# Performance work log

Measured on AMD Instinct MI355X. Metric: run time of the kernel, lower is better.

## Reference

```python
import jax, jax.numpy as jnp
import numpy as np

NUM_NODES = 50000
NUM_HYPEREDGES = 20000
NNZ = 1600000
IN_DIM = 256
OUT_DIM = 128


def setup_inputs() -> dict:
    key = jax.random.key(0)
    k1, k2, k3, k4, k5 = jax.random.split(key, 5)
    x = jax.random.normal(k1, (NUM_NODES, IN_DIM), dtype=jnp.float32)
    node_idx = jax.random.randint(k2, (NNZ,), 0, NUM_NODES)
    edge_idx = jax.random.randint(k3, (NNZ,), 0, NUM_HYPEREDGES)
    hyperedge_index = jnp.stack([node_idx, edge_idx], axis=0)  # [2, nnz]
    # glorot-style init for HypergraphConv's internal Linear (bias=False)
    scale = np.sqrt(6.0 / (IN_DIM + OUT_DIM)).astype(np.float32)
    lin_weight = jax.random.uniform(k4, (IN_DIM, OUT_DIM), dtype=jnp.float32,
                                    minval=-scale, maxval=scale)
    bias = jnp.zeros((OUT_DIM,), dtype=jnp.float32)
    return {"x_node_features": x, "lin_weight": lin_weight, "bias": bias,
            "hyperedge_index": hyperedge_index}


def reference(x_node_features, lin_weight, bias, hyperedge_index):
    src = hyperedge_index[0]   # node ids   [nnz]
    edge = hyperedge_index[1]  # hyperedge ids [nnz]
    ones = jnp.ones_like(src, dtype=x_node_features.dtype)

    # X Theta
    xw = x_node_features @ lin_weight  # [N, F_out]

    # D^{-1}: node degree (hyperedge weights default to 1)
    deg_n = jax.ops.segment_sum(ones, src, num_segments=NUM_NODES)
    d_inv = jnp.where(deg_n > 0, 1.0 / deg_n, 0.0)
    # B^{-1}: hyperedge cardinality
    deg_e = jax.ops.segment_sum(ones, edge, num_segments=NUM_HYPEREDGES)
    b_inv = jnp.where(deg_e > 0, 1.0 / deg_e, 0.0)

    # node -> hyperedge: m_e = B_e^{-1} * sum_{i in e} (X Theta)_i
    m_e = jax.ops.segment_sum(xw[src], edge, num_segments=NUM_HYPEREDGES)
    m_e = m_e * b_inv[:, None]  # [E, F_out]

    # hyperedge -> node: out_i = D_i^{-1} * sum_{e ni i} m_e
    out = jax.ops.segment_sum(m_e[edge], src, num_segments=NUM_NODES)
    out = out * d_inv[:, None] + bias  # [N, F_out]

    # ReLU + mean pool over nodes
    return jnp.mean(jax.nn.relu(out), axis=0)  # [F_out]
```

## Files before the change

kernel.cpp:

```cpp
#include <hip/hip_runtime.h>

#define NUM_N 50000
#define NUM_E 20000
#define IN_DIM 256
#define OUT_DIM 128
#define NBE 1250
#define NBN 1563
#define NCLS 8
#define ECAPC 256
#define NCAPC 192
#define SCAT_CHUNK 4096
#define NGEMM 782
#define XSCALE 16.0f

typedef unsigned short ushort_t;
typedef unsigned int uint_t;
typedef __attribute__((ext_vector_type(8))) short short8_t;
typedef __attribute__((ext_vector_type(4))) float f32x4_t;

__device__ __forceinline__ int clamp8(int q) { return min(max(q, -127), 127); }
__device__ __forceinline__ int lo8(uint_t u) { return (int)(signed char)(u & 0xff); }
__device__ __forceinline__ int hi8(uint_t u) { return ((int)(short)(ushort_t)u) >> 8; }
__device__ __forceinline__ ushort_t f2bf(float f) {
    uint_t u = __float_as_uint(f);
    u += 0x7fffu + ((u >> 16) & 1u);
    return (ushort_t)(u >> 16);
}

__global__ void init_kernel(int* __restrict__ gcur_e, int* __restrict__ gcur_n,
                            float* __restrict__ macc) {
    int t = blockIdx.x * 1024 + threadIdx.x;
    if (t < NCLS * NBE) gcur_e[t] = t * ECAPC;
    if (t < NCLS * NBN) gcur_n[t] = t * NCAPC;
    if (t < 128) macc[t] = 0.f;
}

__global__ __launch_bounds__(256) void gemm_scatter_kernel(
        const float* __restrict__ x, const float* __restrict__ w,
        char* __restrict__ xw, int nrows,
        const int* __restrict__ node_idx, const int* __restrict__ edge_idx, int nnz,
        int* __restrict__ gcur_e, int* __restrict__ gcur_n,
        uint_t* __restrict__ stag_e, uint_t* __restrict__ stag_n) {
    __shared__ int smem[5632];
    int tid = threadIdx.x;

    if (blockIdx.x >= NGEMM) {
        int* lh    = smem;
        int* lbase = smem + 2813;
        int cls = blockIdx.x & (NCLS - 1);
        int bid = blockIdx.x - NGEMM;
        int nblk = gridDim.x - NGEMM;
        for (int cbase = bid * SCAT_CHUNK; cbase < nnz; cbase += nblk * SCAT_CHUNK) {
            int cend = min(cbase + SCAT_CHUNK, nnz);
            for (int i = tid; i < NBE + NBN; i += 256) lh[i] = 0;
            __syncthreads();
            for (int i = cbase + tid; i < cend; i += 256) {
                atomicAdd(&lh[edge_idx[i] >> 4], 1);
                atomicAdd(&lh[NBE + (node_idx[i] >> 5)], 1);
            }
            __syncthreads();
            for (int i = tid; i < NBE; i += 256) {
                int c = lh[i];
                lbase[i] = c ? atomicAdd(&gcur_e[cls * NBE + i], c) : 0;
            }
            for (int i = tid; i < NBN; i += 256) {
                int c = lh[NBE + i];
                lbase[NBE + i] = c ? atomicAdd(&gcur_n[cls * NBN + i], c) : 0;
            }
            __syncthreads();
            for (int i = tid; i < NBE + NBN; i += 256) lh[i] = 0;
            __syncthreads();
            for (int i = cbase + tid; i < cend; i += 256) {
                int v = node_idx[i];
                int e = edge_idx[i];
                uint_t pk = ((uint_t)v << 16) | (uint_t)e;
                int be = e >> 4;
                int bn = v >> 5;
                int pe = lbase[be] + atomicAdd(&lh[be], 1);
                if (pe < (cls * NBE + be + 1) * ECAPC) stag_e[pe] = pk;
                int pn = lbase[NBE + bn] + atomicAdd(&lh[NBE + bn], 1);
                if (pn < (cls * NBN + bn + 1) * NCAPC) stag_n[pn] = pk;
            }
            __syncthreads();
        }
        return;
    }

    ushort_t* Wt = (ushort_t*)smem;
    int lane = tid & 63;
    int wv = tid >> 6;
    int R = blockIdx.x * 64 + wv * 16;
    int fr = lane & 15;
    int kb = lane >> 4;
    f32x4_t acc[8];
#pragma unroll
    for (int c = 0; c < 8; ++c) acc[c] = (f32x4_t){0.f, 0.f, 0.f, 0.f};
    int arow = min(R + fr, nrows - 1);
    const float* ap = x + (size_t)arow * IN_DIM + kb * 8;

    for (int k0 = 0; k0 < IN_DIM; k0 += 32) {
        __syncthreads();
        {
            int tk = tid >> 3;
            int tc = (tid & 7) * 16;
            const float* wp = w + (size_t)(k0 + tk) * OUT_DIM + tc;
            float4 w0 = *(const float4*)(wp + 0);
            float4 w1 = *(const float4*)(wp + 4);
            float4 w2 = *(const float4*)(wp + 8);
            float4 w3 = *(const float4*)(wp + 12);
            float wvv[16] = {w0.x, w0.y, w0.z, w0.w, w1.x, w1.y, w1.z, w1.w,
                             w2.x, w2.y, w2.z, w2.w, w3.x, w3.y, w3.z, w3.w};
#pragma unroll
            for (int i = 0; i < 16; ++i)
                Wt[(tc + i) * 40 + tk] = f2bf(wvv[i]);
        }
        __syncthreads();
        float4 a0 = *(const float4*)(ap + k0);
        float4 a1 = *(const float4*)(ap + k0 + 4);
        short8_t af;
        af[0] = (short)f2bf(a0.x); af[1] = (short)f2bf(a0.y);
        af[2] = (short)f2bf(a0.z); af[3] = (short)f2bf(a0.w);
        af[4] = (short)f2bf(a1.x); af[5] = (short)f2bf(a1.y);
        af[6] = (short)f2bf(a1.z); af[7] = (short)f2bf(a1.w);
#pragma unroll
        for (int c = 0; c < 8; ++c) {
            short8_t bf = *(short8_t*)&Wt[(c * 16 + fr) * 40 + kb * 8];
            acc[c] = __builtin_amdgcn_mfma_f32_16x16x32_bf16(af, bf, acc[c], 0, 0, 0);
        }
    }
#pragma unroll
    for (int c = 0; c < 8; ++c) {
#pragma unroll
        for (int j = 0; j < 4; ++j) {
            int row = R + kb * 4 + j;
            if (row < nrows) {
                int q = clamp8(__float2int_rn(acc[c][j] * XSCALE));
                xw[(size_t)row * OUT_DIM + c * 16 + fr] = (char)q;
            }
        }
    }
}

__global__ __launch_bounds__(256) void edge_agg_kernel(const uint_t* __restrict__ stag_e,
                                                       const int* __restrict__ gcur_e,
                                                       const ushort_t* __restrict__ xw16,
                                                       ushort_t* __restrict__ me16) {
    __shared__ int acc[16 * 128];
    __shared__ int cnt[16];
    int tid = threadIdx.x;
    int lane = tid & 63;
    int wid = tid >> 6;
    int b = blockIdx.x;
    for (int i = tid; i < 16 * 128; i += 256) acc[i] = 0;
    if (tid < 16) cnt[tid] = 0;
    __syncthreads();
    for (int cls = 0; cls < NCLS; ++cls) {
        int idx = cls * NBE + b;
        int beg = idx * ECAPC;
        int end = min(gcur_e[idx], beg + ECAPC);
        int cb = beg + wid * 16;
        for (; cb + 16 <= end; cb += 64) {
            uint4 pa = *(const uint4*)&stag_e[cb];
            uint4 pb = *(const uint4*)&stag_e[cb + 4];
            uint4 pc = *(const uint4*)&stag_e[cb + 8];
            uint4 pd = *(const uint4*)&stag_e[cb + 12];
            uint_t pk[16] = {pa.x, pa.y, pa.z, pa.w, pb.x, pb.y, pb.z, pb.w,
                             pc.x, pc.y, pc.z, pc.w, pd.x, pd.y, pd.z, pd.w};
            uint_t u[16];
#pragma unroll
            for (int j = 0; j < 16; ++j)
                u[j] = xw16[(size_t)(pk[j] >> 16) * 64 + lane];
#pragma unroll
            for (int j = 0; j < 16; ++j) {
                int r = (pk[j] & 15) * 128;
                atomicAdd(&acc[r + lane],      lo8(u[j]));
                atomicAdd(&acc[r + 64 + lane], hi8(u[j]));
            }
            if (lane == 0) {
#pragma unroll
                for (int j = 0; j < 16; ++j) atomicAdd(&cnt[pk[j] & 15], 1);
            }
        }
        if (cb < end) {
            int m = end - cb;
            uint4 pa = *(const uint4*)&stag_e[cb];
            uint4 pb = *(const uint4*)&stag_e[cb + 4];
            uint4 pc = *(const uint4*)&stag_e[cb + 8];
            uint4 pd = *(const uint4*)&stag_e[cb + 12];
            uint_t pk[16] = {pa.x, pa.y, pa.z, pa.w, pb.x, pb.y, pb.z, pb.w,
                             pc.x, pc.y, pc.z, pc.w, pd.x, pd.y, pd.z, pd.w};
            uint_t u[16];
#pragma unroll
            for (int j = 0; j < 16; ++j)
                u[j] = xw16[(size_t)(pk[j] >> 16) * 64 + lane];
#pragma unroll
            for (int j = 0; j < 16; ++j) {
                bool ok = j < m;
                int r = (pk[j] & 15) * 128;
                atomicAdd(&acc[r + lane],      ok ? lo8(u[j]) : 0);
                atomicAdd(&acc[r + 64 + lane], ok ? hi8(u[j]) : 0);
            }
            if (lane == 0) {
#pragma unroll
                for (int j = 0; j < 16; ++j)
                    if (j < m) atomicAdd(&cnt[pk[j] & 15], 1);
            }
        }
    }
    __syncthreads();
    for (int r = wid; r < 16; r += 4) {
        int e = b * 16 + r;
        int c = cnt[r];
        float f = c ? 4.0f / (float)c : 0.f;
        int q0 = clamp8(__float2int_rn((float)acc[r * 128 + lane] * f));
        int q1 = clamp8(__float2int_rn((float)acc[r * 128 + 64 + lane] * f));
        me16[(size_t)e * 64 + lane] = (ushort_t)((q0 & 0xff) | ((q1 & 0xff) << 8));
    }
}

__global__ __launch_bounds__(256) void node_agg_kernel(const uint_t* __restrict__ stag_n,
                                                       const int* __restrict__ gcur_n,
                                                       const ushort_t* __restrict__ me16,
                                                       const float* __restrict__ bias,
                                                       float* __restrict__ mean_acc) {
    __shared__ int acc[32 * 128];
    __shared__ int cnt[32];
    int tid = threadIdx.x;
    int lane = tid & 63;
    int wid = tid >> 6;
    int b = blockIdx.x;
    for (int i = tid; i < 32 * 128; i += 256) acc[i] = 0;
    if (tid < 32) cnt[tid] = 0;
    __syncthreads();
    for (int cls = 0; cls < NCLS; ++cls) {
        int idx = cls * NBN + b;
        int beg = idx * NCAPC;
        int end = min(gcur_n[idx], beg + NCAPC);
        int cb = beg + wid * 16;
        for (; cb + 16 <= end; cb += 64) {
            uint4 pa = *(const uint4*)&stag_n[cb];
            uint4 pb = *(const uint4*)&stag_n[cb + 4];
            uint4 pc = *(const uint4*)&stag_n[cb + 8];
            uint4 pd = *(const uint4*)&stag_n[cb + 12];
            uint_t pk[16] = {pa.x, pa.y, pa.z, pa.w, pb.x, pb.y, pb.z, pb.w,
                             pc.x, pc.y, pc.z, pc.w, pd.x, pd.y, pd.z, pd.w};
            uint_t u[16];
#pragma unroll
            for (int j = 0; j < 16; ++j)
                u[j] = me16[(size_t)(pk[j] & 0xffff) * 64 + lane];
#pragma unroll
            for (int j = 0; j < 16; ++j) {
                int r = ((pk[j] >> 16) & 31) * 128;
                atomicAdd(&acc[r + lane],      lo8(u[j]));
                atomicAdd(&acc[r + 64 + lane], hi8(u[j]));
            }
            if (lane == 0) {
#pragma unroll
                for (int j = 0; j < 16; ++j) atomicAdd(&cnt[(pk[j] >> 16) & 31], 1);
            }
        }
        if (cb < end) {
            int m = end - cb;
            uint4 pa = *(const uint4*)&stag_n[cb];
            uint4 pb = *(const uint4*)&stag_n[cb + 4];
            uint4 pc = *(const uint4*)&stag_n[cb + 8];
            uint4 pd = *(const uint4*)&stag_n[cb + 12];
            uint_t pk[16] = {pa.x, pa.y, pa.z, pa.w, pb.x, pb.y, pb.z, pb.w,
                             pc.x, pc.y, pc.z, pc.w, pd.x, pd.y, pd.z, pd.w};
            uint_t u[16];
#pragma unroll
            for (int j = 0; j < 16; ++j)
                u[j] = me16[(size_t)(pk[j] & 0xffff) * 64 + lane];
#pragma unroll
            for (int j = 0; j < 16; ++j) {
                bool ok = j < m;
                int r = ((pk[j] >> 16) & 31) * 128;
                atomicAdd(&acc[r + lane],      ok ? lo8(u[j]) : 0);
                atomicAdd(&acc[r + 64 + lane], ok ? hi8(u[j]) : 0);
            }
            if (lane == 0) {
#pragma unroll
                for (int j = 0; j < 16; ++j)
                    if (j < m) atomicAdd(&cnt[(pk[j] >> 16) & 31], 1);
            }
        }
    }
    __syncthreads();
    if (tid < 128) {
        int c = tid;
        int sw = (c & 1) ? (64 + (c >> 1)) : (c >> 1);
        float bc = bias[c];
        float s = 0.f;
        int nmax = min(32, NUM_N - b * 32);
        for (int r = 0; r < nmax; ++r) {
            int cc = cnt[r];
            float dinv = cc ? 1.0f / (64.0f * (float)cc) : 0.f;
            s += fmaxf((float)acc[r * 128 + sw] * dinv + bc, 0.f);
        }
        atomicAdd(&mean_acc[c], s);
    }
}

__global__ void finalize_kernel(const float* __restrict__ mean_acc, float* __restrict__ out) {
    int t = threadIdx.x;
    if (t < 128) out[t] = mean_acc[t] * (1.0f / (float)NUM_N);
}

extern "C" void kernel_launch(void* const* d_in, const int* in_sizes, int n_in,
                              void* d_out, int out_size, void* d_ws, size_t ws_size,
                              hipStream_t stream) {
    const float* x    = (const float*)d_in[0];
    const float* w    = (const float*)d_in[1];
    const float* bias = (const float*)d_in[2];
    const int*   hei  = (const int*)d_in[3];
    int nnz = in_sizes[3] / 2;
    const int* node_idx = hei;
    const int* edge_idx = hei + nnz;
    float* out = (float*)d_out;

    char* ws = (char*)d_ws;
    char*     xw     = ws;
    ushort_t* me16   = (ushort_t*)(ws + 6400000);
    uint_t*   stag_e = (uint_t*)(ws + 8960000);
    uint_t*   stag_n = (uint_t*)(ws + 19200064);
    int* gcur_e = (int*)(ws + 28803200);
    int* gcur_n = (int*)(ws + 28843200);
    float* macc = (float*)(ws + 28893216);

    int nscat = (nnz + SCAT_CHUNK - 1) / SCAT_CHUNK;

    init_kernel<<<13, 1024, 0, stream>>>(gcur_e, gcur_n, macc);
    gemm_scatter_kernel<<<NGEMM + nscat, 256, 0, stream>>>(
        x, w, xw, NUM_N, node_idx, edge_idx, nnz, gcur_e, gcur_n, stag_e, stag_n);

    edge_agg_kernel<<<NBE, 256, 0, stream>>>(stag_e, gcur_e, (const ushort_t*)xw, me16);
    node_agg_kernel<<<NBN, 256, 0, stream>>>(stag_n, gcur_n, me16, bias, macc);
    finalize_kernel<<<1, 128, 0, stream>>>(macc, out);
}
```

Measured before the change: 196.9 us.

## Halve node bucket size and pack scatter histogram counters into 16-bit halves

```diff
diff --git a/kernel.cpp b/kernel.cpp
--- a/kernel.cpp
+++ b/kernel.cpp
@@ -5,10 +5,11 @@
 #define IN_DIM 256
 #define OUT_DIM 128
 #define NBE 1250
-#define NBN 1563
+#define NBN 3125
+#define NB_TOT (NBE + NBN)
 #define NCLS 8
 #define ECAPC 256
-#define NCAPC 192
+#define NCAPC 128
 #define SCAT_CHUNK 4096
 #define NGEMM 782
 #define XSCALE 16.0f
@@ -41,44 +42,48 @@
         const int* __restrict__ node_idx, const int* __restrict__ edge_idx, int nnz,
         int* __restrict__ gcur_e, int* __restrict__ gcur_n,
         uint_t* __restrict__ stag_e, uint_t* __restrict__ stag_n) {
-    __shared__ int smem[5632];
+    __shared__ int smem[6564];
     int tid = threadIdx.x;
 
     if (blockIdx.x >= NGEMM) {
-        int* lh    = smem;
-        int* lbase = smem + 2813;
+        int* lbase = smem;
+        int* lhp   = smem + NB_TOT;
         int cls = blockIdx.x & (NCLS - 1);
         int bid = blockIdx.x - NGEMM;
         int nblk = gridDim.x - NGEMM;
         for (int cbase = bid * SCAT_CHUNK; cbase < nnz; cbase += nblk * SCAT_CHUNK) {
             int cend = min(cbase + SCAT_CHUNK, nnz);
-            for (int i = tid; i < NBE + NBN; i += 256) lh[i] = 0;
+            for (int i = tid; i < (NB_TOT + 1) / 2; i += 256) lhp[i] = 0;
             __syncthreads();
             for (int i = cbase + tid; i < cend; i += 256) {
-                atomicAdd(&lh[edge_idx[i] >> 4], 1);
-                atomicAdd(&lh[NBE + (node_idx[i] >> 5)], 1);
-            }
-            __syncthreads();
-            for (int i = tid; i < NBE; i += 256) {
-                int c = lh[i];
-                lbase[i] = c ? atomicAdd(&gcur_e[cls * NBE + i], c) : 0;
-            }
-            for (int i = tid; i < NBN; i += 256) {
-                int c = lh[NBE + i];
-                lbase[NBE + i] = c ? atomicAdd(&gcur_n[cls * NBN + i], c) : 0;
-            }
-            __syncthreads();
-            for (int i = tid; i < NBE + NBN; i += 256) lh[i] = 0;
+                int be = edge_idx[i] >> 4;
+                atomicAdd(&lhp[be >> 1], 1 << ((be & 1) * 16));
+                int bn = NBE + (node_idx[i] >> 4);
+                atomicAdd(&lhp[bn >> 1], 1 << ((bn & 1) * 16));
+            }
+            __syncthreads();
+            for (int i = tid; i < NB_TOT; i += 256) {
+                int c = (lhp[i >> 1] >> ((i & 1) * 16)) & 0xffff;
+                if (i < NBE)
+                    lbase[i] = c ? atomicAdd(&gcur_e[cls * NBE + i], c) : 0;
+                else
+                    lbase[i] = c ? atomicAdd(&gcur_n[cls * NBN + (i - NBE)], c) : 0;
+            }
+            __syncthreads();
+            for (int i = tid; i < (NB_TOT + 1) / 2; i += 256) lhp[i] = 0;
             __syncthreads();
             for (int i = cbase + tid; i < cend; i += 256) {
                 int v = node_idx[i];
                 int e = edge_idx[i];
                 uint_t pk = ((uint_t)v << 16) | (uint_t)e;
                 int be = e >> 4;
-                int bn = v >> 5;
-                int pe = lbase[be] + atomicAdd(&lh[be], 1);
+                uint_t prev = (uint_t)atomicAdd(&lhp[be >> 1], 1 << ((be & 1) * 16));
+                int pe = lbase[be] + (int)((prev >> ((be & 1) * 16)) & 0xffff);
                 if (pe < (cls * NBE + be + 1) * ECAPC) stag_e[pe] = pk;
-                int pn = lbase[NBE + bn] + atomicAdd(&lh[NBE + bn], 1);
+                int bn = v >> 4;
+                int bnl = NBE + bn;
+                prev = (uint_t)atomicAdd(&lhp[bnl >> 1], 1 << ((bnl & 1) * 16));
+                int pn = lbase[bnl] + (int)((prev >> ((bnl & 1) * 16)) & 0xffff);
                 if (pn < (cls * NBN + bn + 1) * NCAPC) stag_n[pn] = pk;
             }
             __syncthreads();
@@ -223,14 +228,14 @@
                                                        const ushort_t* __restrict__ me16,
                                                        const float* __restrict__ bias,
                                                        float* __restrict__ mean_acc) {
-    __shared__ int acc[32 * 128];
-    __shared__ int cnt[32];
+    __shared__ int acc[16 * 128];
+    __shared__ int cnt[16];
     int tid = threadIdx.x;
     int lane = tid & 63;
     int wid = tid >> 6;
     int b = blockIdx.x;
-    for (int i = tid; i < 32 * 128; i += 256) acc[i] = 0;
-    if (tid < 32) cnt[tid] = 0;
+    for (int i = tid; i < 16 * 128; i += 256) acc[i] = 0;
+    if (tid < 16) cnt[tid] = 0;
     __syncthreads();
     for (int cls = 0; cls < NCLS; ++cls) {
         int idx = cls * NBN + b;
@@ -250,13 +255,13 @@
                 u[j] = me16[(size_t)(pk[j] & 0xffff) * 64 + lane];
 #pragma unroll
             for (int j = 0; j < 16; ++j) {
-                int r = ((pk[j] >> 16) & 31) * 128;
+                int r = ((pk[j] >> 16) & 15) * 128;
                 atomicAdd(&acc[r + lane],      lo8(u[j]));
                 atomicAdd(&acc[r + 64 + lane], hi8(u[j]));
             }
             if (lane == 0) {
 #pragma unroll
-                for (int j = 0; j < 16; ++j) atomicAdd(&cnt[(pk[j] >> 16) & 31], 1);
+                for (int j = 0; j < 16; ++j) atomicAdd(&cnt[(pk[j] >> 16) & 15], 1);
             }
         }
         if (cb < end) {
@@ -274,14 +279,14 @@
 #pragma unroll
             for (int j = 0; j < 16; ++j) {
                 bool ok = j < m;
-                int r = ((pk[j] >> 16) & 31) * 128;
+                int r = ((pk[j] >> 16) & 15) * 128;
                 atomicAdd(&acc[r + lane],      ok ? lo8(u[j]) : 0);
                 atomicAdd(&acc[r + 64 + lane], ok ? hi8(u[j]) : 0);
             }
             if (lane == 0) {
 #pragma unroll
                 for (int j = 0; j < 16; ++j)
-                    if (j < m) atomicAdd(&cnt[(pk[j] >> 16) & 31], 1);
+                    if (j < m) atomicAdd(&cnt[(pk[j] >> 16) & 15], 1);
             }
         }
     }
@@ -291,8 +296,7 @@
         int sw = (c & 1) ? (64 + (c >> 1)) : (c >> 1);
         float bc = bias[c];
         float s = 0.f;
-        int nmax = min(32, NUM_N - b * 32);
-        for (int r = 0; r < nmax; ++r) {
+        for (int r = 0; r < 16; ++r) {
             int cc = cnt[r];
             float dinv = cc ? 1.0f / (64.0f * (float)cc) : 0.f;
             s += fmaxf((float)acc[r * 128 + sw] * dinv + bc, 0.f);
@@ -323,13 +327,13 @@
     ushort_t* me16   = (ushort_t*)(ws + 6400000);
     uint_t*   stag_e = (uint_t*)(ws + 8960000);
     uint_t*   stag_n = (uint_t*)(ws + 19200064);
-    int* gcur_e = (int*)(ws + 28803200);
-    int* gcur_n = (int*)(ws + 28843200);
-    float* macc = (float*)(ws + 28893216);
+    int* gcur_e = (int*)(ws + 32000128);
+    int* gcur_n = (int*)(ws + 32040128);
+    float* macc = (float*)(ws + 32140128);
 
     int nscat = (nnz + SCAT_CHUNK - 1) / SCAT_CHUNK;
 
-    init_kernel<<<13, 1024, 0, stream>>>(gcur_e, gcur_n, macc);
+    init_kernel<<<25, 1024, 0, stream>>>(gcur_e, gcur_n, macc);
     gemm_scatter_kernel<<<NGEMM + nscat, 256, 0, stream>>>(
         x, w, xw, NUM_N, node_idx, edge_idx, nnz, gcur_e, gcur_n, stag_e, stag_n);
 
```

After: 233.5 us. 1.19x slower.
